# Performance work log

Measured on AMD Instinct MI355X. Metric: run time of the kernel, lower is better.

## Reference

```python
import jax, jax.numpy as jnp
import numpy as np

B, S, ENC, DEC, ATTN = 64, 2048, 512, 512, 256

def setup_inputs() -> dict:
    key = jax.random.key(0)
    k1, k2, k3, k4, k5 = jax.random.split(key, 5)
    s = 0.05
    return {
        "enc_outputs": jax.random.normal(k1, (B, S, ENC), dtype=jnp.float32),
        "dec_state": jax.random.normal(k2, (B, DEC), dtype=jnp.float32),
        "W_enc": jax.random.normal(k3, (ENC, ATTN), dtype=jnp.float32) * s,
        "W_dec": jax.random.normal(k4, (DEC, ATTN), dtype=jnp.float32) * s,
        "v": jax.random.normal(k5, (ATTN,), dtype=jnp.float32) * s,
    }

def reference(enc_outputs, dec_state, W_enc, W_dec, v):
    # enc_proj: [B,S,A], dec_proj: [B,1,A]
    enc_proj = jnp.einsum('bse,ea->bsa', enc_outputs, W_enc)
    dec_proj = jnp.einsum('bd,da->ba', dec_state, W_dec)[:, None, :]
    scores = jnp.einsum('bsa,a->bs', jnp.tanh(enc_proj + dec_proj), v)  # [B,S]
    attn_weights = jax.nn.softmax(scores, axis=-1)
    context = jnp.einsum('bs,bse->be', attn_weights, enc_outputs)  # [B,ENC]
    return (context, attn_weights)
```

## Files before the change

kernel.cpp:

```cpp
#include <hip/hip_runtime.h>
#include <hip/hip_bf16.h>
#include <stdint.h>

#define B_    64
#define S_    2048
#define ENC_  512
#define ATTN_ 256

typedef __bf16 bf16;
typedef bf16  bf16x8 __attribute__((ext_vector_type(8)));
typedef float f32x4  __attribute__((ext_vector_type(4)));

__device__ __forceinline__ float fexp2(float x) {
#if __has_builtin(__builtin_amdgcn_exp2f)
    return __builtin_amdgcn_exp2f(x);
#else
    return exp2f(x);
#endif
}
__device__ __forceinline__ float frcp(float x) {
#if __has_builtin(__builtin_amdgcn_rcpf)
    return __builtin_amdgcn_rcpf(x);
#else
    return 1.0f / x;
#endif
}
__device__ __forceinline__ float fast_tanh(float x) {
    float e = fexp2(x * 2.8853900817779268f);
    return 1.0f - 2.0f * frcp(e + 1.0f);
}

__device__ __forceinline__ void async_copy16(const void* g, void* l) {
#if __has_builtin(__builtin_amdgcn_global_load_lds)
    __builtin_amdgcn_global_load_lds(
        (__attribute__((address_space(1))) void*)(g),
        (__attribute__((address_space(3))) void*)(l), 16, 0, 0);
#else
    *(uint4*)l = *(const uint4*)g;
#endif
}

__global__ __launch_bounds__(256) void k_setup(const float* __restrict__ W_enc,
                                               const float* __restrict__ dec_state,
                                               const float* __restrict__ W_dec,
                                               bf16* __restrict__ WT,
                                               float* __restrict__ dp) {
    int blk = blockIdx.x;
    if (blk < 512) {
        int idx = blk * 256 + threadIdx.x;
        int n = idx >> 9;
        int k = idx & 511;
        WT[idx] = (bf16)W_enc[k * ATTN_ + n];
    } else {
        int b = blk - 512;
        int a = threadIdx.x;
        const float* ds = dec_state + b * 512;
        float acc = 0.f;
#pragma unroll 8
        for (int d = 0; d < 512; ++d)
            acc += ds[d] * W_dec[d * ATTN_ + a];
        dp[b * ATTN_ + a] = acc;
    }
}

__global__ __launch_bounds__(256, 2) void k_scores(
    const float* __restrict__ enc,
    const bf16*  __restrict__ WT,
    const float* __restrict__ dp,
    const float* __restrict__ v,
    float* __restrict__ out_scores)
{
    __shared__ __align__(16) bf16 As[128 * 40];
    __shared__ __align__(16) bf16 Bs[256 * 32];
    __shared__ float partial[4][64];

    const int tid  = threadIdx.x;
    const int wave = tid >> 6;
    const int lane = tid & 63;
    const int l15  = lane & 15;
    const int q    = lane >> 4;
    const int m0   = blockIdx.x * 128;
    const int b    = blockIdx.x >> 4;

    const int mrow0 = (wave >> 1) * 64;
    const int ncol0 = (wave & 1) * 128;

    float dpv[8], vv[8];
#pragma unroll
    for (int nt = 0; nt < 8; ++nt) {
        int col = ncol0 + nt * 16 + l15;
        dpv[nt] = dp[b * 256 + col];
        vv[nt]  = v[col];
    }

    const f32x4 zero4 = {0.f, 0.f, 0.f, 0.f};
    f32x4 acc[4][8];
#pragma unroll
    for (int mt = 0; mt < 4; ++mt)
#pragma unroll
        for (int nt = 0; nt < 8; ++nt)
            acc[mt][nt] = zero4;

    const int arow = tid >> 1;
    const int akc  = tid & 1;
    const float* ag = enc + (size_t)(m0 + arow) * 512 + akc * 16;
    bf16* as_dst = &As[arow * 40 + akc * 16];

    const int bcol4 = tid >> 2;
    const int bslot = tid & 3;

    for (int ks = 0; ks < 16; ++ks) {
#pragma unroll
        for (int r = 0; r < 4; ++r) {
            int c = r * 64 + bcol4;
            int g = bslot ^ ((c + (c >> 2)) & 3);
            async_copy16(WT + (size_t)c * 512 + ks * 32 + g * 8,
                         &Bs[r * 2048 + tid * 8]);
        }
        {
            const float* s = ag + ks * 32;
            float4 f0 = *(const float4*)(s);
            float4 f1 = *(const float4*)(s + 4);
            float4 f2 = *(const float4*)(s + 8);
            float4 f3 = *(const float4*)(s + 12);
            bf16x8 lo, hi;
            lo[0]=(bf16)f0.x; lo[1]=(bf16)f0.y; lo[2]=(bf16)f0.z; lo[3]=(bf16)f0.w;
            lo[4]=(bf16)f1.x; lo[5]=(bf16)f1.y; lo[6]=(bf16)f1.z; lo[7]=(bf16)f1.w;
            hi[0]=(bf16)f2.x; hi[1]=(bf16)f2.y; hi[2]=(bf16)f2.z; hi[3]=(bf16)f2.w;
            hi[4]=(bf16)f3.x; hi[5]=(bf16)f3.y; hi[6]=(bf16)f3.z; hi[7]=(bf16)f3.w;
            *(bf16x8*)(as_dst)     = lo;
            *(bf16x8*)(as_dst + 8) = hi;
        }
        __syncthreads();

        bf16x8 af[4];
#pragma unroll
        for (int mt = 0; mt < 4; ++mt) {
            int row = mrow0 + mt * 16 + l15;
            af[mt] = *(const bf16x8*)(&As[row * 40 + q * 8]);
        }
        bf16x8 bfr[8];
#pragma unroll
        for (int nt = 0; nt < 8; ++nt) {
            int col = ncol0 + nt * 16 + l15;
            int p = q ^ ((col + (col >> 2)) & 3);
            bfr[nt] = *(const bf16x8*)(&Bs[col * 32 + p * 8]);
        }
#pragma unroll
        for (int mt = 0; mt < 4; ++mt)
#pragma unroll
            for (int nt = 0; nt < 8; ++nt)
                acc[mt][nt] = __builtin_amdgcn_mfma_f32_16x16x32_bf16(af[mt], bfr[nt], acc[mt][nt], 0, 0, 0);
        __syncthreads();
    }

#pragma unroll
    for (int mt = 0; mt < 4; ++mt) {
#pragma unroll
        for (int r = 0; r < 4; ++r) {
            float s = 0.f;
#pragma unroll
            for (int nt = 0; nt < 8; ++nt)
                s += fast_tanh(acc[mt][nt][r] + dpv[nt]) * vv[nt];
            s += __shfl_xor(s, 1, 16);
            s += __shfl_xor(s, 2, 16);
            s += __shfl_xor(s, 4, 16);
            s += __shfl_xor(s, 8, 16);
            if (l15 == 0)
                partial[wave][mt * 16 + q * 4 + r] = s;
        }
    }
    __syncthreads();
    if (tid < 128) {
        int mw   = tid >> 6;
        int rloc = tid & 63;
        out_scores[m0 + mw * 64 + rloc] =
            partial[mw * 2][rloc] + partial[mw * 2 + 1][rloc];
    }
}

__global__ __launch_bounds__(256) void k_softmax(float* __restrict__ attn) {
    int b = blockIdx.x;
    float* s = attn + b * 2048;
    __shared__ float red[256];
    int tid = threadIdx.x;

    float x[8];
    float mx = -1e30f;
#pragma unroll
    for (int i = 0; i < 8; ++i) { x[i] = s[tid + 256 * i]; mx = fmaxf(mx, x[i]); }
    red[tid] = mx;
    __syncthreads();
    for (int off = 128; off > 0; off >>= 1) {
        if (tid < off) red[tid] = fmaxf(red[tid], red[tid + off]);
        __syncthreads();
    }
    mx = red[0];
    __syncthreads();

    float e[8];
    float lsum = 0.f;
#pragma unroll
    for (int i = 0; i < 8; ++i) { e[i] = fexp2((x[i] - mx) * 1.4426950408889634f); lsum += e[i]; }
    red[tid] = lsum;
    __syncthreads();
    for (int off = 128; off > 0; off >>= 1) {
        if (tid < off) red[tid] += red[tid + off];
        __syncthreads();
    }
    float inv = 1.0f / red[0];
#pragma unroll
    for (int i = 0; i < 8; ++i) s[tid + 256 * i] = e[i] * inv;
}

__global__ __launch_bounds__(256) void k_context(const float* __restrict__ enc,
                                                 const float* __restrict__ attn,
                                                 float* __restrict__ partial) {
    int b    = blockIdx.x >> 3;
    int slab = blockIdx.x & 7;
    int tid  = threadIdx.x;
    int eq   = tid & 127;
    int sr   = tid >> 7;
    const float* eb = enc + ((size_t)b * 2048 + slab * 256) * 512;
    const float* w  = attn + b * 2048 + slab * 256;

    f32x4 acc = {0.f, 0.f, 0.f, 0.f};
#pragma unroll 4
    for (int s = sr; s < 256; s += 2) {
        float ws = w[s];
        f32x4 ev = *(const f32x4*)(eb + (size_t)s * 512 + eq * 4);
        acc += ev * ws;
    }
    __shared__ f32x4 red[128];
    if (sr) red[eq] = acc;
    __syncthreads();
    if (!sr) {
        acc += red[eq];
        *(f32x4*)(partial + (size_t)blockIdx.x * 512 + eq * 4) = acc;
    }
}

__global__ __launch_bounds__(128) void k_ctxred(const float* __restrict__ partial,
                                                float* __restrict__ ctx) {
    int b  = blockIdx.x;
    int eq = threadIdx.x;
    f32x4 a = {0.f, 0.f, 0.f, 0.f};
#pragma unroll
    for (int slab = 0; slab < 8; ++slab)
        a += *(const f32x4*)(partial + ((size_t)b * 8 + slab) * 512 + eq * 4);
    *(f32x4*)(ctx + b * 512 + eq * 4) = a;
}

extern "C" void kernel_launch(void* const* d_in, const int* in_sizes, int n_in,
                              void* d_out, int out_size, void* d_ws, size_t ws_size,
                              hipStream_t stream) {
    const float* enc       = (const float*)d_in[0];
    const float* dec_state = (const float*)d_in[1];
    const float* W_enc     = (const float*)d_in[2];
    const float* W_dec     = (const float*)d_in[3];
    const float* v         = (const float*)d_in[4];

    float* ctx  = (float*)d_out;
    float* attn = (float*)d_out + 64 * 512;

    char*  ws      = (char*)d_ws;
    bf16*  WT      = (bf16*)ws;
    float* dp      = (float*)(ws + 256 * 1024);
    float* partial = (float*)(ws + 256 * 1024 + 64 * 1024);

    k_setup  <<<576, 256, 0, stream>>>(W_enc, dec_state, W_dec, WT, dp);
    k_scores <<<1024, 256, 0, stream>>>(enc, WT, dp, v, attn);
    k_softmax<<<64, 256, 0, stream>>>(attn);
    k_context<<<512, 256, 0, stream>>>(enc, attn, partial);
    k_ctxred <<<64, 128, 0, stream>>>(partial, ctx);
}
```

Baseline: 449.1 us.

## Double-buffer score GEMM staging and fuse softmax with context via atomics

The scores GEMM now double-buffers its A and B shared-memory tiles, so loads for the next k-step are issued before the current step's MFMAs and only one barrier per step remains. Softmax, context accumulation and the partial reduction are merged into one kernel with 1024 blocks. Each block recomputes the full-row softmax, writes its 128-element slice of weights, and atomically adds its context partial into the output, which the setup kernel now zeroes. This removes two launches and the partial-buffer round trip. The cost is a redundant softmax per block, float atomics with a nondeterministic summation order, and more shared memory in the scores kernel, which may affect occupancy.

```diff
diff --git a/kernel.cpp b/kernel.cpp
--- a/kernel.cpp
+++ b/kernel.cpp
@@ -44,7 +44,8 @@
                                                const float* __restrict__ dec_state,
                                                const float* __restrict__ W_dec,
                                                bf16* __restrict__ WT,
-                                               float* __restrict__ dp) {
+                                               float* __restrict__ dp,
+                                               float* __restrict__ ctx) {
     int blk = blockIdx.x;
     if (blk < 512) {
         int idx = blk * 256 + threadIdx.x;
@@ -54,12 +55,24 @@
     } else {
         int b = blk - 512;
         int a = threadIdx.x;
+        *(float2*)(ctx + b * 512 + a * 2) = make_float2(0.f, 0.f);
         const float* ds = dec_state + b * 512;
         float acc = 0.f;
 #pragma unroll 8
         for (int d = 0; d < 512; ++d)
             acc += ds[d] * W_dec[d * ATTN_ + a];
         dp[b * ATTN_ + a] = acc;
+    }
+}
+
+__device__ __forceinline__ void stage_b(const bf16* __restrict__ WT, bf16* bsbuf,
+                                        int ks, int bcol4, int bslot, int tid) {
+#pragma unroll
+    for (int r = 0; r < 4; ++r) {
+        int c = r * 64 + bcol4;
+        int g = bslot ^ ((c + (c >> 2)) & 3);
+        async_copy16(WT + (size_t)c * 512 + ks * 32 + g * 8,
+                     bsbuf + r * 2048 + tid * 8);
     }
 }
 
@@ -70,8 +83,8 @@
     const float* __restrict__ v,
     float* __restrict__ out_scores)
 {
-    __shared__ __align__(16) bf16 As[128 * 40];
-    __shared__ __align__(16) bf16 Bs[256 * 32];
+    __shared__ __align__(16) bf16 As[2][128 * 40];
+    __shared__ __align__(16) bf16 Bs[2][256 * 32];
     __shared__ float partial[4][64];
 
     const int tid  = threadIdx.x;
@@ -85,14 +98,6 @@
     const int mrow0 = (wave >> 1) * 64;
     const int ncol0 = (wave & 1) * 128;
 
-    float dpv[8], vv[8];
-#pragma unroll
-    for (int nt = 0; nt < 8; ++nt) {
-        int col = ncol0 + nt * 16 + l15;
-        dpv[nt] = dp[b * 256 + col];
-        vv[nt]  = v[col];
-    }
-
     const f32x4 zero4 = {0.f, 0.f, 0.f, 0.f};
     f32x4 acc[4][8];
 #pragma unroll
@@ -104,56 +109,82 @@
     const int arow = tid >> 1;
     const int akc  = tid & 1;
     const float* ag = enc + (size_t)(m0 + arow) * 512 + akc * 16;
-    bf16* as_dst = &As[arow * 40 + akc * 16];
+    const int aoff = arow * 40 + akc * 16;
 
     const int bcol4 = tid >> 2;
     const int bslot = tid & 3;
 
+    {
+        float4 f0 = *(const float4*)(ag);
+        float4 f1 = *(const float4*)(ag + 4);
+        float4 f2 = *(const float4*)(ag + 8);
+        float4 f3 = *(const float4*)(ag + 12);
+        stage_b(WT, Bs[0], 0, bcol4, bslot, tid);
+        bf16x8 lo, hi;
+        lo[0]=(bf16)f0.x; lo[1]=(bf16)f0.y; lo[2]=(bf16)f0.z; lo[3]=(bf16)f0.w;
+        lo[4]=(bf16)f1.x; lo[5]=(bf16)f1.y; lo[6]=(bf16)f1.z; lo[7]=(bf16)f1.w;
+        hi[0]=(bf16)f2.x; hi[1]=(bf16)f2.y; hi[2]=(bf16)f2.z; hi[3]=(bf16)f2.w;
+        hi[4]=(bf16)f3.x; hi[5]=(bf16)f3.y; hi[6]=(bf16)f3.z; hi[7]=(bf16)f3.w;
+        *(bf16x8*)(&As[0][aoff])     = lo;
+        *(bf16x8*)(&As[0][aoff + 8]) = hi;
+    }
+    __syncthreads();
+
     for (int ks = 0; ks < 16; ++ks) {
-#pragma unroll
-        for (int r = 0; r < 4; ++r) {
-            int c = r * 64 + bcol4;
-            int g = bslot ^ ((c + (c >> 2)) & 3);
-            async_copy16(WT + (size_t)c * 512 + ks * 32 + g * 8,
-                         &Bs[r * 2048 + tid * 8]);
-        }
-        {
-            const float* s = ag + ks * 32;
-            float4 f0 = *(const float4*)(s);
-            float4 f1 = *(const float4*)(s + 4);
-            float4 f2 = *(const float4*)(s + 8);
-            float4 f3 = *(const float4*)(s + 12);
+        const int cur = ks & 1;
+        const bf16* Asc = As[cur];
+        const bf16* Bsc = Bs[cur];
+
+        bf16x8 af[4];
+#pragma unroll
+        for (int mt = 0; mt < 4; ++mt) {
+            int row = mrow0 + mt * 16 + l15;
+            af[mt] = *(const bf16x8*)(Asc + row * 40 + q * 8);
+        }
+        bf16x8 bfr[8];
+#pragma unroll
+        for (int nt = 0; nt < 8; ++nt) {
+            int col = ncol0 + nt * 16 + l15;
+            int p = q ^ ((col + (col >> 2)) & 3);
+            bfr[nt] = *(const bf16x8*)(Bsc + col * 32 + p * 8);
+        }
+
+        float4 f0, f1, f2, f3;
+        if (ks < 15) {
+            const float* s = ag + (ks + 1) * 32;
+            f0 = *(const float4*)(s);
+            f1 = *(const float4*)(s + 4);
+            f2 = *(const float4*)(s + 8);
+            f3 = *(const float4*)(s + 12);
+            stage_b(WT, Bs[cur ^ 1], ks + 1, bcol4, bslot, tid);
+        }
+
+#pragma unroll
+        for (int mt = 0; mt < 4; ++mt)
+#pragma unroll
+            for (int nt = 0; nt < 8; ++nt)
+                acc[mt][nt] = __builtin_amdgcn_mfma_f32_16x16x32_bf16(af[mt], bfr[nt], acc[mt][nt], 0, 0, 0);
+
+        if (ks < 15) {
             bf16x8 lo, hi;
             lo[0]=(bf16)f0.x; lo[1]=(bf16)f0.y; lo[2]=(bf16)f0.z; lo[3]=(bf16)f0.w;
             lo[4]=(bf16)f1.x; lo[5]=(bf16)f1.y; lo[6]=(bf16)f1.z; lo[7]=(bf16)f1.w;
             hi[0]=(bf16)f2.x; hi[1]=(bf16)f2.y; hi[2]=(bf16)f2.z; hi[3]=(bf16)f2.w;
             hi[4]=(bf16)f3.x; hi[5]=(bf16)f3.y; hi[6]=(bf16)f3.z; hi[7]=(bf16)f3.w;
-            *(bf16x8*)(as_dst)     = lo;
-            *(bf16x8*)(as_dst + 8) = hi;
+            bf16* dst = &As[cur ^ 1][aoff];
+            *(bf16x8*)(dst)     = lo;
+            *(bf16x8*)(dst + 8) = hi;
         }
         __syncthreads();
-
-        bf16x8 af[4];
-#pragma unroll
-        for (int mt = 0; mt < 4; ++mt) {
-            int row = mrow0 + mt * 16 + l15;
-            af[mt] = *(const bf16x8*)(&As[row * 40 + q * 8]);
-        }
-        bf16x8 bfr[8];
-#pragma unroll
-        for (int nt = 0; nt < 8; ++nt) {
-            int col = ncol0 + nt * 16 + l15;
-            int p = q ^ ((col + (col >> 2)) & 3);
-            bfr[nt] = *(const bf16x8*)(&Bs[col * 32 + p * 8]);
-        }
-#pragma unroll
-        for (int mt = 0; mt < 4; ++mt)
-#pragma unroll
-            for (int nt = 0; nt < 8; ++nt)
-                acc[mt][nt] = __builtin_amdgcn_mfma_f32_16x16x32_bf16(af[mt], bfr[nt], acc[mt][nt], 0, 0, 0);
-        __syncthreads();
-    }
-
+    }
+
+    float dpv[8], vv[8];
+#pragma unroll
+    for (int nt = 0; nt < 8; ++nt) {
+        int col = ncol0 + nt * 16 + l15;
+        dpv[nt] = dp[b * 256 + col];
+        vv[nt]  = v[col];
+    }
 #pragma unroll
     for (int mt = 0; mt < 4; ++mt) {
 #pragma unroll
@@ -179,16 +210,23 @@
     }
 }
 
-__global__ __launch_bounds__(256) void k_softmax(float* __restrict__ attn) {
-    int b = blockIdx.x;
-    float* s = attn + b * 2048;
+__global__ __launch_bounds__(256) void k_ctx(const float* __restrict__ enc,
+                                             const float* __restrict__ scores,
+                                             float* __restrict__ attn,
+                                             float* __restrict__ ctx) {
     __shared__ float red[256];
-    int tid = threadIdx.x;
+    __shared__ float wlds[128];
+    __shared__ f32x4 vred[128];
+
+    const int tid  = threadIdx.x;
+    const int b    = blockIdx.x >> 4;
+    const int slab = blockIdx.x & 15;
+    const float* sc = scores + b * 2048;
 
     float x[8];
     float mx = -1e30f;
 #pragma unroll
-    for (int i = 0; i < 8; ++i) { x[i] = s[tid + 256 * i]; mx = fmaxf(mx, x[i]); }
+    for (int i = 0; i < 8; ++i) { x[i] = sc[tid + 256 * i]; mx = fmaxf(mx, x[i]); }
     red[tid] = mx;
     __syncthreads();
     for (int off = 128; off > 0; off >>= 1) {
@@ -209,46 +247,46 @@
         __syncthreads();
     }
     float inv = 1.0f / red[0];
-#pragma unroll
-    for (int i = 0; i < 8; ++i) s[tid + 256 * i] = e[i] * inv;
-}
-
-__global__ __launch_bounds__(256) void k_context(const float* __restrict__ enc,
-                                                 const float* __restrict__ attn,
-                                                 float* __restrict__ partial) {
-    int b    = blockIdx.x >> 3;
-    int slab = blockIdx.x & 7;
-    int tid  = threadIdx.x;
-    int eq   = tid & 127;
-    int sr   = tid >> 7;
-    const float* eb = enc + ((size_t)b * 2048 + slab * 256) * 512;
-    const float* w  = attn + b * 2048 + slab * 256;
+
+#pragma unroll
+    for (int i = 0; i < 8; ++i) {
+        int idx = tid + 256 * i;
+        int r   = idx - slab * 128;
+        if ((unsigned)r < 128u) {
+            float w = e[i] * inv;
+            attn[b * 2048 + idx] = w;
+            wlds[r] = w;
+        }
+    }
+    __syncthreads();
+
+    const int eq = tid & 127;
+    const int sr = tid >> 7;
+    const float* eb = enc + ((size_t)b * 2048 + slab * 128) * 512;
 
     f32x4 acc = {0.f, 0.f, 0.f, 0.f};
-#pragma unroll 4
-    for (int s = sr; s < 256; s += 2) {
-        float ws = w[s];
-        f32x4 ev = *(const f32x4*)(eb + (size_t)s * 512 + eq * 4);
-        acc += ev * ws;
-    }
-    __shared__ f32x4 red[128];
-    if (sr) red[eq] = acc;
+    for (int g = 0; g < 8; ++g) {
+        const int sbase = g * 16 + sr * 8;
+        f32x4 ev[8];
+        float wv[8];
+#pragma unroll
+        for (int j = 0; j < 8; ++j) {
+            ev[j] = *(const f32x4*)(eb + (size_t)(sbase + j) * 512 + eq * 4);
+            wv[j] = wlds[sbase + j];
+        }
+#pragma unroll
+        for (int j = 0; j < 8; ++j) acc += ev[j] * wv[j];
+    }
+    if (sr) vred[eq] = acc;
     __syncthreads();
     if (!sr) {
-        acc += red[eq];
-        *(f32x4*)(partial + (size_t)blockIdx.x * 512 + eq * 4) = acc;
-    }
-}
-
-__global__ __launch_bounds__(128) void k_ctxred(const float* __restrict__ partial,
-                                                float* __restrict__ ctx) {
-    int b  = blockIdx.x;
-    int eq = threadIdx.x;
-    f32x4 a = {0.f, 0.f, 0.f, 0.f};
-#pragma unroll
-    for (int slab = 0; slab < 8; ++slab)
-        a += *(const f32x4*)(partial + ((size_t)b * 8 + slab) * 512 + eq * 4);
-    *(f32x4*)(ctx + b * 512 + eq * 4) = a;
+        acc += vred[eq];
+        float* cp = ctx + b * 512 + eq * 4;
+        atomicAdd(cp + 0, acc[0]);
+        atomicAdd(cp + 1, acc[1]);
+        atomicAdd(cp + 2, acc[2]);
+        atomicAdd(cp + 3, acc[3]);
+    }
 }
 
 extern "C" void kernel_launch(void* const* d_in, const int* in_sizes, int n_in,
@@ -263,14 +301,12 @@
     float* ctx  = (float*)d_out;
     float* attn = (float*)d_out + 64 * 512;
 
-    char*  ws      = (char*)d_ws;
-    bf16*  WT      = (bf16*)ws;
-    float* dp      = (float*)(ws + 256 * 1024);
-    float* partial = (float*)(ws + 256 * 1024 + 64 * 1024);
-
-    k_setup  <<<576, 256, 0, stream>>>(W_enc, dec_state, W_dec, WT, dp);
-    k_scores <<<1024, 256, 0, stream>>>(enc, WT, dp, v, attn);
-    k_softmax<<<64, 256, 0, stream>>>(attn);
-    k_context<<<512, 256, 0, stream>>>(enc, attn, partial);
-    k_ctxred <<<64, 128, 0, stream>>>(partial, ctx);
-}
+    char*  ws     = (char*)d_ws;
+    bf16*  WT     = (bf16*)ws;
+    float* dp     = (float*)(ws + 256 * 1024);
+    float* scores = (float*)(ws + 256 * 1024 + 64 * 1024);
+
+    k_setup <<<576, 256, 0, stream>>>(W_enc, dec_state, W_dec, WT, dp, ctx);
+    k_scores<<<1024, 256, 0, stream>>>(enc, WT, dp, v, scores);
+    k_ctx   <<<1024, 256, 0, stream>>>(enc, scores, attn, ctx);
+}
```

Result: no change. 446.7 us (-0.5%).
